# Performance work log

Hardware: AMD Instinct MI355X
Metric: run time of the kernel (lower is better)

The kernel has to match this reference:

```python
import jax, jax.numpy as jnp
import numpy as np

B, S, H, L = 64, 512, 768, 9


def setup_inputs() -> dict:
    key = jax.random.key(0)
    k0, k1, k2, k3, k4, k5, k6 = jax.random.split(key, 7)
    hidden = jax.random.normal(k0, (B, S, H), dtype=jnp.float32)
    W = jax.random.normal(k1, (L, H), dtype=jnp.float32) * 0.02
    b = jnp.zeros((L,), dtype=jnp.float32)
    start_transitions = jax.random.uniform(k2, (L,), minval=-0.1, maxval=0.1)
    end_transitions = jax.random.uniform(k3, (L,), minval=-0.1, maxval=0.1)
    transitions = jax.random.uniform(k4, (L, L), minval=-0.1, maxval=0.1)
    # variable-length sequences (position 0 always valid), like real padded batches
    lens = jax.random.randint(k5, (B,), S // 2, S + 1)
    attention_mask = jnp.arange(S)[None, :] < lens[:, None]  # (B,S) bool
    labels = jax.random.randint(k6, (B, S), 0, L).astype(jnp.int32)
    return dict(hidden=hidden, W=W, b=b, start_transitions=start_transitions,
                end_transitions=end_transitions, transitions=transitions,
                labels=labels, attention_mask=attention_mask)


def _crf_neg_log_likelihood(feats, labels, mask, start, end, trans):
    """feats (B,S,L) emissions; labels (B,S) int; mask (B,S) bool. Returns scalar mean NLL."""
    fdt = feats.dtype
    # ---- log denominator: forward algorithm as a scan over time ----
    fT = jnp.swapaxes(feats, 0, 1)  # (S,B,L)
    mT = jnp.swapaxes(mask, 0, 1)   # (S,B)
    alpha0 = start + fT[0]          # (B,L)

    def step(alpha, xs):
        f_t, m_t = xs
        # (B,L_prev,1) + (L_prev,L_next) + (B,1,L_next) -> logsumexp over prev
        new = jax.nn.logsumexp(alpha[:, :, None] + trans[None, :, :] + f_t[:, None, :], axis=1)
        return jnp.where(m_t[:, None], new, alpha), None

    alpha, _ = jax.lax.scan(step, alpha0, (fT[1:], mT[1:]))
    log_den = jax.nn.logsumexp(alpha + end, axis=1)  # (B,)

    # ---- log numerator: score of the gold path, fully vectorized ----
    emit = jnp.take_along_axis(feats, labels[..., None].astype(jnp.int32), axis=2)[..., 0]  # (B,S)
    tr = trans[labels[:, :-1], labels[:, 1:]]  # (B,S-1)
    score = start[labels[:, 0]] + emit[:, 0]
    score = score + jnp.sum((tr + emit[:, 1:]) * mask[:, 1:].astype(fdt), axis=1)
    lens = jnp.sum(mask.astype(jnp.int32), axis=1) - 1  # index of last valid token
    last_tags = jnp.take_along_axis(labels, lens[:, None], axis=1)[:, 0]
    score = score + end[last_tags]

    return jnp.mean(log_den - score)


def reference(hidden, W, b, start_transitions, end_transitions, transitions, labels, attention_mask):
    # hidden2label linear (dropout is identity in eval mode)
    feats = jnp.einsum('bsh,lh->bsl', hidden, W) + b  # (B,S,L)
    return _crf_neg_log_likelihood(feats, labels, attention_mask,
                                   start_transitions, end_transitions, transitions)
```

## Files before the change

kernel.cpp:

```cpp
#include <hip/hip_runtime.h>
#include <hip/hip_bf16.h>

#define BB 64
#define SS 512
#define HH 768
#define LL 9
#define CL 8
#define NC (SS / CL)
#define NEG (-1e30f)

#define EXP2F(x) exp2f(x)
#define LOG2F(x) __log2f(x)

static __device__ __forceinline__ float dot4(float4 a, float4 b) {
    return a.x * b.x + a.y * b.y + a.z * b.z + a.w * b.w;
}

static __device__ __forceinline__ float max9(const float* v) {
    float m1 = fmaxf(fmaxf(v[0], v[1]), v[2]);
    float m2 = fmaxf(fmaxf(v[3], v[4]), v[5]);
    float m3 = fmaxf(fmaxf(v[6], v[7]), v[8]);
    return fmaxf(fmaxf(m1, m2), m3);
}

static __device__ __forceinline__ float sum9exp(const float* v, float mx) {
    float e0 = EXP2F(v[0] - mx), e1 = EXP2F(v[1] - mx), e2 = EXP2F(v[2] - mx);
    float e3 = EXP2F(v[3] - mx), e4 = EXP2F(v[4] - mx), e5 = EXP2F(v[5] - mx);
    float e6 = EXP2F(v[6] - mx), e7 = EXP2F(v[7] - mx), e8 = EXP2F(v[8] - mx);
    return ((e0 + e1) + (e2 + e3)) + (((e4 + e5) + (e6 + e7)) + e8);
}

template <int CTRL>
static __device__ __forceinline__ float dpp_add(float v) {
    return v + __int_as_float(
        __builtin_amdgcn_update_dpp(0, __float_as_int(v), CTRL, 0xF, 0xF, true));
}

static __device__ __forceinline__ float group_sum16(float v) {
    v = dpp_add<0xB1>(v);
    v = dpp_add<0x4E>(v);
    v = dpp_add<0x124>(v);
    v = dpp_add<0x128>(v);
    return v;
}

static __device__ __forceinline__ float lds_sum4(const float* p) {
    float4 q = *(const float4*)p;
    return (q.x + q.y) + (q.z + q.w);
}

__global__ __launch_bounds__(256, 3)
void fused_kernel(const float* __restrict__ hidden,
                  const float* __restrict__ W,
                  const float* __restrict__ bias,
                  const float* __restrict__ start_t,
                  const float* __restrict__ end_t,
                  const float* __restrict__ trans,
                  const int* __restrict__ labels,
                  const int* __restrict__ mask,
                  float* __restrict__ Q,
                  float* __restrict__ A0,
                  float* __restrict__ Sc,
                  float* __restrict__ out0) {
    const int bid  = blockIdx.x;
    const int b    = bid >> 6;
    const int c    = bid & (NC - 1);
    const int tid  = threadIdx.x;
    const int lane = tid & 63;
    const int wv   = tid >> 6;

    if (bid == 0 && tid == 0) out0[0] = 0.f;

    __shared__ float fsl4[CL][LL][4];
    __shared__ float Pb[2][LL][16];

    const int bS     = b * SS;
    const int t_base = c * CL;
    const float INV_LN2 = 1.4426950408889634f;

    const int i  = tid >> 4;
    const int j  = tid & 15;
    const int jc = j < LL ? j : LL - 1;

    float trC[LL];
#pragma unroll
    for (int k = 0; k < LL; ++k) trC[k] = trans[k * LL + jc] * INV_LN2;
    const float bjc = bias[jc];

    const int off   = (c == 0) ? 1 : 0;
    const int steps = CL - off;
    const int t0    = t_base + off;

    int na = 0;
#pragma unroll
    for (int u = 0; u < CL; ++u)
        na += (u < steps && mask[bS + t0 + u] != 0) ? 1 : 0;

    int mt = 0, lc = 0, lp = 0, mnext = 0;
    const int t_sc = t_base + lane;
    if (wv == 3 && lane < CL) {
        mt    = mask[bS + t_sc];
        lc    = labels[bS + t_sc];
        lp    = (t_sc >= 1) ? labels[bS + t_sc - 1] : 0;
        mnext = (t_sc == SS - 1) ? 0 : mask[bS + t_sc + 1];
    }

    float4 wreg[3][LL];
#pragma unroll
    for (int c3 = 0; c3 < 3; ++c3)
#pragma unroll
        for (int l = 0; l < LL; ++l)
            wreg[c3][l] = *(const float4*)(W + l * HH + c3 * 256 + (lane << 2));

    const float* hbase = hidden + ((size_t)bS + t_base) * HH;
    const int r0 = wv * 2, r1 = r0 + 1;
    const float4* h0p = (const float4*)(hbase + (size_t)r0 * HH);
    const float4* h1p = (const float4*)(hbase + (size_t)r1 * HH);
    float4 a0 = h0p[lane], a1 = h0p[64 + lane], a2 = h0p[128 + lane];
    float4 b0 = h1p[lane], b1 = h1p[64 + lane], b2 = h1p[128 + lane];

    float accA[LL], accB[LL];
#pragma unroll
    for (int l = 0; l < LL; ++l) {
        accA[l] = dot4(a0, wreg[0][l]) + dot4(a1, wreg[1][l]) + dot4(a2, wreg[2][l]);
        accB[l] = dot4(b0, wreg[0][l]) + dot4(b1, wreg[1][l]) + dot4(b2, wreg[2][l]);
    }

    const int g  = lane >> 4;
    const int sl = lane & 15;
    float selA = 0.f, selB = 0.f;
#pragma unroll
    for (int l = 0; l < LL; ++l) {
        float rA = group_sum16(accA[l]);
        float rB = group_sum16(accB[l]);
        if (sl == l) { selA = rA; selB = rB; }
    }
    if (sl < LL) {
        fsl4[r0][sl][g] = selA;
        fsl4[r1][sl][g] = selB;
    }

    float P = (i == j) ? 0.f : NEG;
    if (tid < 144) Pb[0][i][j] = P;
    __syncthreads();

    if (wv == 3 && lane < CL) {
        float sc = 0.f;
        if (t_sc >= 1 && mt)
            sc += trans[lp * LL + lc] + lds_sum4(&fsl4[lane][lc][0]) + bias[lc];
        if (t_sc == 0)
            sc += start_t[lc] + lds_sum4(&fsl4[0][lc][0]) + bias[lc];
        if (mt && !mnext) sc += end_t[lc];
#pragma unroll
        for (int o = 1; o < CL; o <<= 1) sc += __shfl_xor(sc, o);
        if (lane == 0) Sc[bid] = sc;
    }
    if (c == 0 && wv == 2 && lane < LL)
        A0[b * 16 + lane] =
            (start_t[lane] + lds_sum4(&fsl4[0][lane][0]) + bias[lane]) * INV_LN2;

    float fsr[CL];
#pragma unroll
    for (int u = 0; u < CL; ++u)
        fsr[u] = (u < steps) ? (lds_sum4(&fsl4[u + off][jc][0]) + bjc) * INV_LN2 : 0.f;

#pragma unroll
    for (int s = 0; s < CL; ++s) {
        if (s < na) {
            if (tid < 144) {
                const float* row = &Pb[s & 1][i][0];
                float v[LL];
#pragma unroll
                for (int k = 0; k < LL; ++k) v[k] = row[k] + trC[k];
                const float mx  = max9(v);
                const float sum = sum9exp(v, mx);
                P = mx + LOG2F(sum) + fsr[s];
                Pb[(s + 1) & 1][i][j] = P;
            }
        }
        __syncthreads();
    }

    if (tid < 144 && j < LL)
        Q[(size_t)bid * (LL * LL) + i * LL + j] = P;
}

__global__ __launch_bounds__(64, 1)
void combine_kernel(const float* __restrict__ Q,
                    const float* __restrict__ A0,
                    const float* __restrict__ Sc,
                    const float* __restrict__ end_t,
                    float* __restrict__ out) {
    const int b    = blockIdx.x;
    const int lane = threadIdx.x;
    const int j    = lane < LL ? lane : LL - 1;
    const float INV_LN2 = 1.4426950408889634f;
    const float LN2     = 0.6931471805599453f;

    float score = Sc[b * NC + lane];
#pragma unroll
    for (int o = 1; o < 64; o <<= 1) score += __shfl_xor(score, o);

    float alpha[LL];
#pragma unroll
    for (int k = 0; k < LL; ++k) alpha[k] = A0[b * 16 + k];

    const float* Qb = Q + (size_t)b * NC * (LL * LL);
    float qcol[LL], qnext[LL];
#pragma unroll
    for (int k = 0; k < LL; ++k) qnext[k] = Qb[k * LL + j];
    for (int cc = 0; cc < NC; ++cc) {
#pragma unroll
        for (int k = 0; k < LL; ++k) qcol[k] = qnext[k];
        if (cc + 1 < NC) {
            const float* Qn = Qb + (size_t)(cc + 1) * (LL * LL);
#pragma unroll
            for (int k = 0; k < LL; ++k) qnext[k] = Qn[k * LL + j];
        }
        float v[LL];
#pragma unroll
        for (int k = 0; k < LL; ++k) v[k] = alpha[k] + qcol[k];
        const float mx  = max9(v);
        const float sum = sum9exp(v, mx);
        const float anew = mx + LOG2F(sum);
#pragma unroll
        for (int k = 0; k < LL; ++k)
            alpha[k] = __uint_as_float(__builtin_amdgcn_readlane(__float_as_uint(anew), k));
    }

    float v[LL];
#pragma unroll
    for (int k = 0; k < LL; ++k) v[k] = alpha[k] + end_t[k] * INV_LN2;
    const float mx  = max9(v);
    const float sum = sum9exp(v, mx);
    const float log_den = (mx + LOG2F(sum)) * LN2;

    if (lane == 0)
        atomicAdd(out, (log_den - score) * (1.0f / BB));
}

extern "C" void kernel_launch(void* const* d_in, const int* in_sizes, int n_in,
                              void* d_out, int out_size, void* d_ws, size_t ws_size,
                              hipStream_t stream) {
    const float* hidden = (const float*)d_in[0];
    const float* W      = (const float*)d_in[1];
    const float* bias   = (const float*)d_in[2];
    const float* startT = (const float*)d_in[3];
    const float* endT   = (const float*)d_in[4];
    const float* trans  = (const float*)d_in[5];
    const int*   labels = (const int*)d_in[6];
    const int*   mask   = (const int*)d_in[7];

    float* Q  = (float*)d_ws;
    float* A0 = Q + (size_t)BB * NC * LL * LL;
    float* Sc = A0 + BB * 16;

    fused_kernel<<<dim3(BB * NC), dim3(256), 0, stream>>>(
        hidden, W, bias, startT, endT, trans, labels, mask, Q, A0, Sc, (float*)d_out);
    combine_kernel<<<dim3(BB), dim3(64), 0, stream>>>(Q, A0, Sc, endT, (float*)d_out);
}
```

Measured before the change: 191.7 us.

## Run chunk transfer-matrix recurrence in one wavefront with register rows, no barriers

The per-chunk log-semiring matrix product now runs in wave 0 alone, with each of 9 lanes holding a full row of P and the whole scaled transition matrix in registers. The per-step shared-memory ping-pong and block-wide __syncthreads are removed. Emission sums are precomputed once into a small LDS table by other waves, and the occupancy hint in launch_bounds is dropped. In exchange, each active lane does 9x more serial work per step, only 9 lanes are active, and register pressure rises.

```diff
diff --git a/kernel.cpp b/kernel.cpp
--- a/kernel.cpp
+++ b/kernel.cpp
@@ -49,7 +49,7 @@
     return (q.x + q.y) + (q.z + q.w);
 }
 
-__global__ __launch_bounds__(256, 3)
+__global__ __launch_bounds__(256)
 void fused_kernel(const float* __restrict__ hidden,
                   const float* __restrict__ W,
                   const float* __restrict__ bias,
@@ -72,20 +72,11 @@
     if (bid == 0 && tid == 0) out0[0] = 0.f;
 
     __shared__ float fsl4[CL][LL][4];
-    __shared__ float Pb[2][LL][16];
+    __shared__ float fsl2[CL][12];
 
     const int bS     = b * SS;
     const int t_base = c * CL;
     const float INV_LN2 = 1.4426950408889634f;
-
-    const int i  = tid >> 4;
-    const int j  = tid & 15;
-    const int jc = j < LL ? j : LL - 1;
-
-    float trC[LL];
-#pragma unroll
-    for (int k = 0; k < LL; ++k) trC[k] = trans[k * LL + jc] * INV_LN2;
-    const float bjc = bias[jc];
 
     const int off   = (c == 0) ? 1 : 0;
     const int steps = CL - off;
@@ -139,50 +130,71 @@
         fsl4[r0][sl][g] = selA;
         fsl4[r1][sl][g] = selB;
     }
-
-    float P = (i == j) ? 0.f : NEG;
-    if (tid < 144) Pb[0][i][j] = P;
+    __syncthreads();
+
+    float T2[LL][LL];
+    if (wv == 0) {
+#pragma unroll
+        for (int k = 0; k < LL; ++k)
+#pragma unroll
+            for (int j = 0; j < LL; ++j)
+                T2[k][j] = trans[k * LL + j] * INV_LN2;
+    } else if (wv <= 2) {
+        const int local = tid - 64;
+        if (local < CL * LL) {
+            const int u  = local / LL;
+            const int jj = local - u * LL;
+            fsl2[u][jj] = lds_sum4(&fsl4[u][jj][0]) + bias[jj];
+        }
+    }
     __syncthreads();
 
     if (wv == 3 && lane < CL) {
         float sc = 0.f;
-        if (t_sc >= 1 && mt)
-            sc += trans[lp * LL + lc] + lds_sum4(&fsl4[lane][lc][0]) + bias[lc];
-        if (t_sc == 0)
-            sc += start_t[lc] + lds_sum4(&fsl4[0][lc][0]) + bias[lc];
-        if (mt && !mnext) sc += end_t[lc];
+        if (t_sc >= 1 && mt) sc += trans[lp * LL + lc] + fsl2[lane][lc];
+        if (t_sc == 0)       sc += start_t[lc] + fsl2[0][lc];
+        if (mt && !mnext)    sc += end_t[lc];
 #pragma unroll
         for (int o = 1; o < CL; o <<= 1) sc += __shfl_xor(sc, o);
         if (lane == 0) Sc[bid] = sc;
     }
-    if (c == 0 && wv == 2 && lane < LL)
-        A0[b * 16 + lane] =
-            (start_t[lane] + lds_sum4(&fsl4[0][lane][0]) + bias[lane]) * INV_LN2;
-
-    float fsr[CL];
-#pragma unroll
-    for (int u = 0; u < CL; ++u)
-        fsr[u] = (u < steps) ? (lds_sum4(&fsl4[u + off][jc][0]) + bjc) * INV_LN2 : 0.f;
+    if (wv == 1 && c == 0 && lane < LL)
+        A0[b * 16 + lane] = (start_t[lane] + fsl2[0][lane]) * INV_LN2;
+
+    if (wv != 0) return;
+
+    const int i = lane;
+    if (i >= LL) return;
+
+    float P[LL];
+#pragma unroll
+    for (int j = 0; j < LL; ++j) P[j] = (i == j) ? 0.f : NEG;
 
 #pragma unroll
     for (int s = 0; s < CL; ++s) {
         if (s < na) {
-            if (tid < 144) {
-                const float* row = &Pb[s & 1][i][0];
+            const float* fr = &fsl2[s + off][0];
+            float f0 = fr[0], f1 = fr[1], f2 = fr[2], f3 = fr[3], f4 = fr[4];
+            float f5 = fr[5], f6 = fr[6], f7 = fr[7], f8 = fr[8];
+            float fj[LL] = {f0, f1, f2, f3, f4, f5, f6, f7, f8};
+            float Pn[LL];
+#pragma unroll
+            for (int j = 0; j < LL; ++j) {
                 float v[LL];
 #pragma unroll
-                for (int k = 0; k < LL; ++k) v[k] = row[k] + trC[k];
+                for (int k = 0; k < LL; ++k) v[k] = P[k] + T2[k][j];
                 const float mx  = max9(v);
                 const float sum = sum9exp(v, mx);
-                P = mx + LOG2F(sum) + fsr[s];
-                Pb[(s + 1) & 1][i][j] = P;
+                Pn[j] = mx + LOG2F(sum) + fj[j] * INV_LN2;
             }
+#pragma unroll
+            for (int j = 0; j < LL; ++j) P[j] = Pn[j];
         }
-        __syncthreads();
-    }
-
-    if (tid < 144 && j < LL)
-        Q[(size_t)bid * (LL * LL) + i * LL + j] = P;
+    }
+
+    float* Qr = Q + (size_t)bid * (LL * LL) + i * LL;
+#pragma unroll
+    for (int j = 0; j < LL; ++j) Qr[j] = P[j];
 }
 
 __global__ __launch_bounds__(64, 1)
```

After: 232.3 us. 21.2% more time.
